# Optimization experiments

Hardware: AMD Instinct MI355X
Metric: run time of the kernel (lower is better)

## Reference

```python
import jax, jax.numpy as jnp
import numpy as np


def setup_inputs() -> dict:
    key = jax.random.key(0)
    ks = jax.random.split(key, 8)
    b, cin, cout, h, w, t, ssize = 4, 128, 128, 64, 64, 16, 512
    return {
        "x": jax.random.normal(ks[0], (b, cin, h, w, t), jnp.float32),
        "style": jax.random.normal(ks[1], (b, ssize), jnp.float32),
        "noise": jax.random.normal(ks[2], (b, 1, h, w, t), jnp.float32),
        # learned params
        "weight": jax.random.normal(ks[3], (cout, cin, 3, 3, 1), jnp.float32),
        "style_w": jax.random.normal(ks[4], (cin, ssize), jnp.float32) * 0.02,
        "style_b": jax.random.normal(ks[5], (cin,), jnp.float32) * 0.02,
        "noise_param": jax.random.normal(ks[6], (cout, 1, 1, 1), jnp.float32) * 0.1,
        "bias_param": jax.random.normal(ks[7], (cout, 1, 1, 1), jnp.float32) * 0.1,
    }


def reference(x, style, noise, weight, style_w, style_b, noise_param, bias_param):
    # style modulation scale per (batch, in-channel)
    s = style @ style_w.T + style_b                         # [b, cin]
    # Demodulation factor per (b, out). Mathematically identical to building
    # per-sample weights W[o,i,k]*s[b,i] and demodulating, but computed as a
    # tiny contraction instead of materializing [b,out,in,k,k,1] weights.
    sig_inv = jax.lax.rsqrt(
        jnp.einsum('oihwt,bi->bo', weight**2, s**2) + 1e-8)  # [b, cout]
    # Since conv is linear in its input, scaling input channels by s and the
    # output channels by sig_inv equals the grouped per-sample conv.
    x_mod = x * s[:, :, None, None, None]                   # [b, cin, h, w, t]
    y = jax.lax.conv_general_dilated(
        x_mod, weight, window_strides=(1, 1, 1), padding='SAME',
        dimension_numbers=('NCDHW', 'OIDHW', 'NCDHW'))      # [b, cout, h, w, t]
    y = y * sig_inv[:, :, None, None, None]
    # noise_param/bias_param are [cout,1,1,1]; broadcast over (h,w,t)
    return y + noise_param * noise + bias_param
```

## Files before the change

kernel.cpp:

```cpp
#include <hip/hip_runtime.h>
#include <hip/hip_bf16.h>
#include <stdint.h>

typedef __bf16 bf16;
typedef bf16 bf16x8 __attribute__((ext_vector_type(8)));
typedef float f32x4 __attribute__((ext_vector_type(4)));
typedef float f32x16 __attribute__((ext_vector_type(16)));

#define AS1 __attribute__((address_space(1)))
#define AS3 __attribute__((address_space(3)))

__device__ __forceinline__ void async_copy16(const void* g, void* l) {
    __builtin_amdgcn_global_load_lds((const AS1 uint32_t*)(g),
                                     (AS3 uint32_t*)(l), 16, 0, 0);
}

template <int N> __device__ __forceinline__ void waitv();
template <> __device__ __forceinline__ void waitv<0>() { asm volatile("s_waitcnt vmcnt(0)" ::: "memory"); }
template <> __device__ __forceinline__ void waitv<6>() { asm volatile("s_waitcnt vmcnt(6)" ::: "memory"); }
template <> __device__ __forceinline__ void waitv<9>() { asm volatile("s_waitcnt vmcnt(9)" ::: "memory"); }


__global__ void k_style(const float* __restrict__ style, const float* __restrict__ sw,
                        const float* __restrict__ sbias, float* __restrict__ s_out,
                        float* __restrict__ guard) {
    if (blockIdx.x == 0) {
#pragma unroll
        for (int j = 0; j < 4; ++j) guard[threadIdx.x + 256 * j] = 0.f;
    }
    int gw = (blockIdx.x * blockDim.x + threadIdx.x) >> 6;
    int lane = threadIdx.x & 63;
    if (gw >= 512) return;
    int b = gw >> 7, c = gw & 127;
    const float* st = style + b * 512;
    const float* wr = sw + c * 512;
    float a = 0.f;
#pragma unroll
    for (int j = 0; j < 8; ++j) a += st[lane + 64 * j] * wr[lane + 64 * j];
    for (int off = 32; off > 0; off >>= 1) a += __shfl_down(a, off, 64);
    if (lane == 0) s_out[gw] = a + sbias[c];
}

__global__ void k_sig(const float* __restrict__ weight, const float* __restrict__ s,
                      float* __restrict__ sig) {
    int gw = (blockIdx.x * blockDim.x + threadIdx.x) >> 6;
    int lane = threadIdx.x & 63;
    if (gw >= 512) return;
    int b = gw >> 7, o = gw & 127;
    float a = 0.f;
#pragma unroll
    for (int j = 0; j < 2; ++j) {
        int i = lane + 64 * j;
        const float* wr = weight + ((size_t)o * 128 + i) * 9;
        float wsq = 0.f;
#pragma unroll
        for (int t = 0; t < 9; ++t) wsq += wr[t] * wr[t];
        float sv = s[b * 128 + i];
        a += wsq * sv * sv;
    }
    for (int off = 32; off > 0; off >>= 1) a += __shfl_down(a, off, 64);
    if (lane == 0) sig[gw] = rsqrtf(a + 1e-8f);
}

__global__ void k_wt(const float* __restrict__ weight, bf16* __restrict__ wt) {
    int i = blockIdx.x * 256 + threadIdx.x;
    if (i >= 147456) return;
    int j = i & 7;
    int co = (i >> 3) & 127;
    int g = (i >> 10) & 1;
    int tap = (i >> 11) % 9;
    int chunk = (i >> 11) / 9;
    int ci = chunk * 16 + g * 8 + j;
    wt[i] = (bf16)weight[((size_t)co * 128 + ci) * 9 + tap];
}

__global__ void k_xt(const float* __restrict__ x, const float* __restrict__ s,
                     bf16* __restrict__ xt) {
    int E = blockIdx.x * 256 + threadIdx.x;
    int b = E >> 16, e = E & 65535;
    const float* xb = x + (size_t)b * 8388608 + e;
    const float* sb = s + b * 128;
#pragma unroll 4
    for (int g = 0; g < 16; ++g) {
        bf16x8 v;
#pragma unroll
        for (int j = 0; j < 8; ++j)
            v[j] = (bf16)(xb[(size_t)(g * 8 + j) * 65536] * sb[g * 8 + j]);
        *(bf16x8*)(xt + ((((size_t)b * 16 + g) << 16) + e) * 8) = v;
    }
}

__global__ __launch_bounds__(256, 2) void conv_main(
    const bf16* __restrict__ xt, const bf16* __restrict__ wt,
    const float* __restrict__ sig_inv, const float* __restrict__ npar,
    const float* __restrict__ bpar, const float* __restrict__ noise,
    const bf16* __restrict__ guard, float* __restrict__ out) {
    __shared__ bf16 Xr[4][576 * 8];
    __shared__ bf16 Wr[3][768 * 8];

    const int tid = threadIdx.x;
    const int lane = tid & 63;
    const int l31 = lane & 31, lhi = lane >> 5;
    const int wm = (tid >> 6) & 1;
    const int wn = tid >> 7;
    const int w0 = blockIdx.x * 16;
    const int h = blockIdx.y;
    const int b = blockIdx.z;
    const size_t bHW = (size_t)b * 65536;

    auto wslab = [&](int s) {
        int slot = s % 3;
#pragma unroll
        for (int it = 0; it < 3; ++it) {
            int v = it * 256 + tid;
            async_copy16(wt + (size_t)s * 6144 + v * 8, &Wr[slot][v * 8]);
        }
    };

    auto xrow = [&](int g) {
        int slot = g & 3;
        int cg = g / 3, dhg = g - cg * 3;
#pragma unroll
        for (int it = 0; it < 3; ++it) {
            int v0 = it * 256 + tid;
            int v = v0 >= 576 ? v0 - 576 : v0;
            int gg = v / 288;
            int e = v - gg * 288;
            int ha = h - 1 + dhg;
            int wa = w0 - 1 + (e >> 4);
            bool ok = ((unsigned)ha < 64u) & ((unsigned)wa < 64u);
            int E = (ha * 64 + wa) * 16 + (e & 15);
            const bf16* gsrc = ok
                ? xt + ((((size_t)b * 16 + cg * 2 + gg) << 16) + E) * 8
                : guard;
            async_copy16(gsrc, &Xr[slot][v * 8]);
        }
    };

    f32x16 acc[2][4] = {};

    const size_t ebase = bHW + (size_t)h * 1024 + w0 * 16 + wn * 128;
    float ns[4];
#pragma unroll
    for (int nf = 0; nf < 4; ++nf) ns[nf] = noise[ebase + nf * 32 + l31];
    __builtin_amdgcn_sched_barrier(0);

    xrow(0);  wslab(0);  xrow(1);

#define PHASE(c, dh, LIT, DOW, DOX)                                            \
    {                                                                          \
        if (DOW) wslab(3 * (c) + (dh) + 1);                                    \
        if (DOX) xrow(3 * (c) + (dh) + 2);                                     \
        waitv<LIT>();                                                          \
        __builtin_amdgcn_sched_barrier(0);                                     \
        __builtin_amdgcn_s_barrier();                                          \
        const int xs_ = (3 * (c) + (dh)) & 3;                                  \
        _Pragma("unroll")                                                      \
        for (int dw = 0; dw < 3; ++dw) {                                       \
            const bf16* wg =                                                   \
                &Wr[dh][((dw * 2 + lhi) * 128 + wm * 64 + l31) * 8];           \
            bf16x8 a0 = *(const bf16x8*)&wg[0];                                \
            bf16x8 a1 = *(const bf16x8*)&wg[32 * 8];                           \
            const bf16* xb =                                                   \
                &Xr[xs_][(lhi * 288 + dw * 16 + wn * 128 + l31) * 8];          \
            bf16x8 b0 = *(const bf16x8*)&xb[0];                                \
            bf16x8 b1 = *(const bf16x8*)&xb[32 * 8];                           \
            bf16x8 b2 = *(const bf16x8*)&xb[64 * 8];                           \
            bf16x8 b3 = *(const bf16x8*)&xb[96 * 8];                           \
            acc[0][0] = __builtin_amdgcn_mfma_f32_32x32x16_bf16(a0, b0, acc[0][0], 0, 0, 0); \
            acc[0][1] = __builtin_amdgcn_mfma_f32_32x32x16_bf16(a0, b1, acc[0][1], 0, 0, 0); \
            acc[0][2] = __builtin_amdgcn_mfma_f32_32x32x16_bf16(a0, b2, acc[0][2], 0, 0, 0); \
            acc[0][3] = __builtin_amdgcn_mfma_f32_32x32x16_bf16(a0, b3, acc[0][3], 0, 0, 0); \
            acc[1][0] = __builtin_amdgcn_mfma_f32_32x32x16_bf16(a1, b0, acc[1][0], 0, 0, 0); \
            acc[1][1] = __builtin_amdgcn_mfma_f32_32x32x16_bf16(a1, b1, acc[1][1], 0, 0, 0); \
            acc[1][2] = __builtin_amdgcn_mfma_f32_32x32x16_bf16(a1, b2, acc[1][2], 0, 0, 0); \
            acc[1][3] = __builtin_amdgcn_mfma_f32_32x32x16_bf16(a1, b3, acc[1][3], 0, 0, 0); \
        }                                                                      \
    }

    for (int c = 0; c < 7; ++c) {
        PHASE(c, 0, 9, true, true);
        PHASE(c, 1, 9, true, true);
        PHASE(c, 2, 9, true, true);
    }
    PHASE(7, 0, 9, true,  true);
    PHASE(7, 1, 6, true,  false);
    PHASE(7, 2, 0, false, false);
#undef PHASE

#pragma unroll
    for (int fm = 0; fm < 2; ++fm) {
        int cob = wm * 64 + fm * 32 + 4 * lhi;
#pragma unroll
        for (int q = 0; q < 4; ++q) {
            int co4 = cob + 8 * q;
            f32x4 sg = *(const f32x4*)&sig_inv[b * 128 + co4];
            f32x4 np4 = *(const f32x4*)&npar[co4];
            f32x4 bp4 = *(const f32x4*)&bpar[co4];
#pragma unroll
            for (int r = 0; r < 4; ++r) {
                int co = co4 + r;
                float* orow = out + ((size_t)(b * 128 + co) * 64 + h) * 1024 +
                              w0 * 16 + wn * 128;
#pragma unroll
                for (int nf = 0; nf < 4; ++nf) {
                    float v = acc[fm][nf][q * 4 + r];
                    orow[nf * 32 + l31] = v * sg[r] + np4[r] * ns[nf] + bp4[r];
                }
            }
        }
    }
}

__global__ void k_naive(const float* __restrict__ x, const float* __restrict__ weight,
                        const float* __restrict__ s, const float* __restrict__ sig,
                        const float* __restrict__ npar, const float* __restrict__ bpar,
                        const float* __restrict__ noise, float* __restrict__ out) {
    size_t o = (size_t)blockIdx.x * 256 + threadIdx.x;
    int t = o & 15, w = (o >> 4) & 63, h = (o >> 10) & 63;
    int co = (o >> 16) & 127, b = (int)(o >> 23);
    float a = 0.f;
    for (int ci = 0; ci < 128; ++ci) {
        const float* xr = x + (size_t)(b * 128 + ci) * 65536;
        const float* wr = weight + ((size_t)co * 128 + ci) * 9;
        float p = 0.f;
#pragma unroll
        for (int kh = 0; kh < 3; ++kh) {
            int ha = h + kh - 1;
            if ((unsigned)ha >= 64u) continue;
#pragma unroll
            for (int kw = 0; kw < 3; ++kw) {
                int wa = w + kw - 1;
                if ((unsigned)wa >= 64u) continue;
                p += xr[(ha * 64 + wa) * 16 + t] * wr[kh * 3 + kw];
            }
        }
        a += p * s[b * 128 + ci];
    }
    int E = b * 65536 + (h * 64 + w) * 16 + t;
    out[o] = a * sig[b * 128 + co] + npar[co] * noise[E] + bpar[co];
}

extern "C" void kernel_launch(void* const* d_in, const int* in_sizes, int n_in,
                              void* d_out, int out_size, void* d_ws, size_t ws_size,
                              hipStream_t stream) {
    const float* x      = (const float*)d_in[0];
    const float* style  = (const float*)d_in[1];
    const float* noise  = (const float*)d_in[2];
    const float* weight = (const float*)d_in[3];
    const float* sw     = (const float*)d_in[4];
    const float* sb     = (const float*)d_in[5];
    const float* npar   = (const float*)d_in[6];
    const float* bpar   = (const float*)d_in[7];
    float* out = (float*)d_out;

    float* s_buf   = (float*)d_ws;
    float* sig_buf = s_buf + 512;
    float* guard   = (float*)((char*)d_ws + 4096);
    bf16*  wt      = (bf16*)((char*)d_ws + 8192);
    bf16*  xt      = (bf16*)((char*)d_ws + 8192 + 294912);
    const size_t NEED = 8192 + 294912 + 67108864ull;

    k_style<<<dim3(128), dim3(256), 0, stream>>>(style, sw, sb, s_buf, guard);
    k_sig<<<dim3(128), dim3(256), 0, stream>>>(weight, s_buf, sig_buf);
    if (ws_size >= NEED) {
        k_wt<<<dim3(576), dim3(256), 0, stream>>>(weight, wt);
        k_xt<<<dim3(1024), dim3(256), 0, stream>>>(x, s_buf, xt);
        conv_main<<<dim3(4, 64, 4), dim3(256), 0, stream>>>(
            xt, wt, sig_buf, npar, bpar, noise, (const bf16*)guard, out);
    } else {
        k_naive<<<dim3(131072), dim3(256), 0, stream>>>(
            x, weight, s_buf, sig_buf, npar, bpar, noise, out);
    }
}
```

Before: 135.7 us.

## Fuse input conversion into conv kernel and fold style scale into weights

Drops the separate pass that scaled x by the style vector and wrote a bf16 channel-interleaved copy. The conv kernel now loads fp32 x directly into registers, converts to bf16 and stores to LDS, with register prefetch of the next row. The style scale moves into a per-batch modulated bf16 weight tensor, built by k_wt. This removes a large intermediate write and read, at the cost of strided fp32 global loads inside the conv loop, synchronous LDS stores, and one fewer LDS X buffer.

```diff
diff --git a/kernel.cpp b/kernel.cpp
--- a/kernel.cpp
+++ b/kernel.cpp
@@ -16,18 +16,12 @@
 }
 
 template <int N> __device__ __forceinline__ void waitv();
-template <> __device__ __forceinline__ void waitv<0>() { asm volatile("s_waitcnt vmcnt(0)" ::: "memory"); }
-template <> __device__ __forceinline__ void waitv<6>() { asm volatile("s_waitcnt vmcnt(6)" ::: "memory"); }
-template <> __device__ __forceinline__ void waitv<9>() { asm volatile("s_waitcnt vmcnt(9)" ::: "memory"); }
+template <> __device__ __forceinline__ void waitv<0>()  { asm volatile("s_waitcnt vmcnt(0)"  ::: "memory"); }
+template <> __device__ __forceinline__ void waitv<27>() { asm volatile("s_waitcnt vmcnt(27)" ::: "memory"); }
 
 
 __global__ void k_style(const float* __restrict__ style, const float* __restrict__ sw,
-                        const float* __restrict__ sbias, float* __restrict__ s_out,
-                        float* __restrict__ guard) {
-    if (blockIdx.x == 0) {
-#pragma unroll
-        for (int j = 0; j < 4; ++j) guard[threadIdx.x + 256 * j] = 0.f;
-    }
+                        const float* __restrict__ sbias, float* __restrict__ s_out) {
     int gw = (blockIdx.x * blockDim.x + threadIdx.x) >> 6;
     int lane = threadIdx.x & 63;
     if (gw >= 512) return;
@@ -62,40 +56,26 @@
     if (lane == 0) sig[gw] = rsqrtf(a + 1e-8f);
 }
 
-__global__ void k_wt(const float* __restrict__ weight, bf16* __restrict__ wt) {
+__global__ void k_wt(const float* __restrict__ weight, const float* __restrict__ s,
+                     bf16* __restrict__ wt) {
     int i = blockIdx.x * 256 + threadIdx.x;
-    if (i >= 147456) return;
+    if (i >= 589824) return;
     int j = i & 7;
     int co = (i >> 3) & 127;
     int g = (i >> 10) & 1;
     int tap = (i >> 11) % 9;
-    int chunk = (i >> 11) / 9;
+    int cb = (i >> 11) / 9;
+    int chunk = cb & 7, b = cb >> 3;
     int ci = chunk * 16 + g * 8 + j;
-    wt[i] = (bf16)weight[((size_t)co * 128 + ci) * 9 + tap];
-}
-
-__global__ void k_xt(const float* __restrict__ x, const float* __restrict__ s,
-                     bf16* __restrict__ xt) {
-    int E = blockIdx.x * 256 + threadIdx.x;
-    int b = E >> 16, e = E & 65535;
-    const float* xb = x + (size_t)b * 8388608 + e;
-    const float* sb = s + b * 128;
-#pragma unroll 4
-    for (int g = 0; g < 16; ++g) {
-        bf16x8 v;
-#pragma unroll
-        for (int j = 0; j < 8; ++j)
-            v[j] = (bf16)(xb[(size_t)(g * 8 + j) * 65536] * sb[g * 8 + j]);
-        *(bf16x8*)(xt + ((((size_t)b * 16 + g) << 16) + e) * 8) = v;
-    }
+    wt[i] = (bf16)(weight[((size_t)co * 128 + ci) * 9 + tap] * s[b * 128 + ci]);
 }
 
 __global__ __launch_bounds__(256, 2) void conv_main(
-    const bf16* __restrict__ xt, const bf16* __restrict__ wt,
+    const float* __restrict__ x, const bf16* __restrict__ wt,
     const float* __restrict__ sig_inv, const float* __restrict__ npar,
     const float* __restrict__ bpar, const float* __restrict__ noise,
-    const bf16* __restrict__ guard, float* __restrict__ out) {
-    __shared__ bf16 Xr[4][576 * 8];
+    float* __restrict__ out) {
+    __shared__ bf16 Xr[3][576 * 8];
     __shared__ bf16 Wr[3][768 * 8];
 
     const int tid = threadIdx.x;
@@ -107,33 +87,55 @@
     const int h = blockIdx.y;
     const int b = blockIdx.z;
     const size_t bHW = (size_t)b * 65536;
+    const bf16* wb = wt + (size_t)b * 147456;
+
+    float XL[24];
 
     auto wslab = [&](int s) {
         int slot = s % 3;
 #pragma unroll
         for (int it = 0; it < 3; ++it) {
             int v = it * 256 + tid;
-            async_copy16(wt + (size_t)s * 6144 + v * 8, &Wr[slot][v * 8]);
+            async_copy16(wb + (size_t)s * 6144 + v * 8, &Wr[slot][v * 8]);
         }
     };
 
-    auto xrow = [&](int g) {
-        int slot = g & 3;
+    auto xload = [&](int g) {
         int cg = g / 3, dhg = g - cg * 3;
-#pragma unroll
-        for (int it = 0; it < 3; ++it) {
-            int v0 = it * 256 + tid;
+        int ha = h - 1 + dhg;
+#pragma unroll
+        for (int cc = 0; cc < 3; ++cc) {
+            int v0 = cc * 256 + tid;
             int v = v0 >= 576 ? v0 - 576 : v0;
-            int gg = v / 288;
-            int e = v - gg * 288;
-            int ha = h - 1 + dhg;
+            int gg = v / 288, e = v - gg * 288;
             int wa = w0 - 1 + (e >> 4);
             bool ok = ((unsigned)ha < 64u) & ((unsigned)wa < 64u);
             int E = (ha * 64 + wa) * 16 + (e & 15);
-            const bf16* gsrc = ok
-                ? xt + ((((size_t)b * 16 + cg * 2 + gg) << 16) + E) * 8
-                : guard;
-            async_copy16(gsrc, &Xr[slot][v * 8]);
+            int Ec = ok ? E : 0;
+            const AS1 float* xp = (const AS1 float*)x +
+                (((size_t)(b * 128 + cg * 16 + gg * 8)) << 16) + Ec;
+#pragma unroll
+            for (int j = 0; j < 8; ++j) XL[cc * 8 + j] = xp[(size_t)j << 16];
+        }
+    };
+
+    auto xstore = [&](int g) {
+        int dhg = g % 3;
+        int ha = h - 1 + dhg;
+        const bf16 zz = (bf16)0.f;
+        const bf16x8 vz = {zz, zz, zz, zz, zz, zz, zz, zz};
+#pragma unroll
+        for (int cc = 0; cc < 3; ++cc) {
+            int v0 = cc * 256 + tid;
+            int v = v0 >= 576 ? v0 - 576 : v0;
+            int gg = v / 288, e = v - gg * 288;
+            int wa = w0 - 1 + (e >> 4);
+            bool ok = ((unsigned)ha < 64u) & ((unsigned)wa < 64u);
+            bf16x8 vv;
+#pragma unroll
+            for (int j = 0; j < 8; ++j) vv[j] = (bf16)XL[cc * 8 + j];
+            vv = ok ? vv : vz;
+            *(bf16x8*)&Xr[dhg][v * 8] = vv;
         }
     };
 
@@ -145,16 +147,20 @@
     for (int nf = 0; nf < 4; ++nf) ns[nf] = noise[ebase + nf * 32 + l31];
     __builtin_amdgcn_sched_barrier(0);
 
-    xrow(0);  wslab(0);  xrow(1);
-
-#define PHASE(c, dh, LIT, DOW, DOX)                                            \
+    xload(0);
+    wslab(0);
+    __builtin_amdgcn_sched_barrier(0);
+
+#define PHASE(c, dh, LIT, DONEXT)                                              \
     {                                                                          \
-        if (DOW) wslab(3 * (c) + (dh) + 1);                                    \
-        if (DOX) xrow(3 * (c) + (dh) + 2);                                     \
+        if (DONEXT) wslab(3 * (c) + (dh) + 1);                                 \
+        xstore(3 * (c) + (dh));                                                \
+        if (DONEXT) xload(3 * (c) + (dh) + 1);                                 \
+        __builtin_amdgcn_sched_barrier(0);                                     \
         waitv<LIT>();                                                          \
+        asm volatile("s_waitcnt lgkmcnt(0)" ::: "memory");                     \
         __builtin_amdgcn_sched_barrier(0);                                     \
         __builtin_amdgcn_s_barrier();                                          \
-        const int xs_ = (3 * (c) + (dh)) & 3;                                  \
         _Pragma("unroll")                                                      \
         for (int dw = 0; dw < 3; ++dw) {                                       \
             const bf16* wg =                                                   \
@@ -162,7 +168,7 @@
             bf16x8 a0 = *(const bf16x8*)&wg[0];                                \
             bf16x8 a1 = *(const bf16x8*)&wg[32 * 8];                           \
             const bf16* xb =                                                   \
-                &Xr[xs_][(lhi * 288 + dw * 16 + wn * 128 + l31) * 8];          \
+                &Xr[dh][(lhi * 288 + dw * 16 + wn * 128 + l31) * 8];           \
             bf16x8 b0 = *(const bf16x8*)&xb[0];                                \
             bf16x8 b1 = *(const bf16x8*)&xb[32 * 8];                           \
             bf16x8 b2 = *(const bf16x8*)&xb[64 * 8];                           \
@@ -179,13 +185,13 @@
     }
 
     for (int c = 0; c < 7; ++c) {
-        PHASE(c, 0, 9, true, true);
-        PHASE(c, 1, 9, true, true);
-        PHASE(c, 2, 9, true, true);
-    }
-    PHASE(7, 0, 9, true,  true);
-    PHASE(7, 1, 6, true,  false);
-    PHASE(7, 2, 0, false, false);
+        PHASE(c, 0, 27, true);
+        PHASE(c, 1, 27, true);
+        PHASE(c, 2, 27, true);
+    }
+    PHASE(7, 0, 27, true);
+    PHASE(7, 1, 27, true);
+    PHASE(7, 2, 0, false);
 #undef PHASE
 
 #pragma unroll
@@ -256,18 +262,15 @@
 
     float* s_buf   = (float*)d_ws;
     float* sig_buf = s_buf + 512;
-    float* guard   = (float*)((char*)d_ws + 4096);
     bf16*  wt      = (bf16*)((char*)d_ws + 8192);
-    bf16*  xt      = (bf16*)((char*)d_ws + 8192 + 294912);
-    const size_t NEED = 8192 + 294912 + 67108864ull;
-
-    k_style<<<dim3(128), dim3(256), 0, stream>>>(style, sw, sb, s_buf, guard);
+    const size_t NEED = 8192 + 4 * 294912ull;
+
+    k_style<<<dim3(128), dim3(256), 0, stream>>>(style, sw, sb, s_buf);
     k_sig<<<dim3(128), dim3(256), 0, stream>>>(weight, s_buf, sig_buf);
     if (ws_size >= NEED) {
-        k_wt<<<dim3(576), dim3(256), 0, stream>>>(weight, wt);
-        k_xt<<<dim3(1024), dim3(256), 0, stream>>>(x, s_buf, xt);
+        k_wt<<<dim3(2304), dim3(256), 0, stream>>>(weight, s_buf, wt);
         conv_main<<<dim3(4, 64, 4), dim3(256), 0, stream>>>(
-            xt, wt, sig_buf, npar, bpar, noise, (const bf16*)guard, out);
+            x, wt, sig_buf, npar, bpar, noise, out);
     } else {
         k_naive<<<dim3(131072), dim3(256), 0, stream>>>(
             x, weight, s_buf, sig_buf, npar, bpar, noise, out);
```

Result: faster. 112.8 us (-16.9%).
